# Performance work log

Hardware: AMD Instinct MI355X
Metric: run time of the kernel (lower is better)

Reference implementation:

```python
import jax, jax.numpy as jnp
import numpy as np

N = 100000
E = 3200000
D_IN = 256
D_OUT = 256
SMOOTH = 0.5


def setup_inputs() -> dict:
    key = jax.random.key(0)
    k1, k2, k3, k4, k5, k6 = jax.random.split(key, 6)
    x = jax.random.normal(k1, (N, D_IN), dtype=jnp.float32)
    W = jax.random.normal(k2, (D_IN, D_OUT), dtype=jnp.float32) * (1.0 / np.sqrt(D_IN))
    b = jax.random.normal(k3, (D_OUT,), dtype=jnp.float32) * 0.01
    edge_weight = jax.random.uniform(k4, (E,), dtype=jnp.float32)
    edge_row = jax.random.randint(k5, (E,), 0, N, dtype=jnp.int32)
    edge_col = jax.random.randint(k6, (E,), 0, N, dtype=jnp.int32)
    return {"x": x, "W": W, "b": b, "edge_weight": edge_weight,
            "edge_row": edge_row, "edge_col": edge_col}


def reference(x, W, b, edge_weight, edge_row, edge_col):
    # support = Linear(input)
    support = x @ W + b  # [N, D_OUT]
    # A_gcn = adj + I; degrees = column sums of A_gcn (identity contributes +1)
    deg = jax.ops.segment_sum(edge_weight, edge_col, num_segments=N) + 1.0  # [N]
    Dm12 = deg ** -0.5  # D^{-1/2}
    # pre-scale, spmm with A_gcn = adj + I, post-scale
    Y = support * Dm12[:, None]
    Z = jax.ops.segment_sum(edge_weight[:, None] * Y[edge_col], edge_row,
                            num_segments=N) + Y  # +Y is the identity part of A_gcn
    Z = Z * Dm12[:, None]
    # residual blend
    return (Z * SMOOTH + support) / (1.0 + SMOOTH)
```

## Files before the change

### kernel.cpp

```cpp
#include <hip/hip_runtime.h>

#define N_NODES 100000
#define N_EDGES 3200000
#define D 256
#define ELL_W 64
#define NPC_CNT 57344
#define NPART_CNT 2
#define NTOTC 114688
#define NPC_ELL 28672
#define NPART_ELL 4
#define NPC_DEG 57344
#define NPART_DEG 2
#define NSLICE2 128
#define SLICE2_E 25000
#define NSLICE_D 128
#define SLICE_D 25000
#define W_SCALE 32768.0f
#define SMOOTH_A (1.0f/3.0f)
#define SMOOTH_B (2.0f/3.0f)

#define AS1 __attribute__((address_space(1)))
#define AS3 __attribute__((address_space(3)))

typedef __attribute__((ext_vector_type(8))) __bf16 bf16x8;
typedef __attribute__((ext_vector_type(4))) float f32x4;
typedef __attribute__((ext_vector_type(2))) float f32x2;

__device__ __forceinline__ unsigned short f2bf(float f) {
    unsigned int u = __float_as_uint(f);
    u = (u + 0x7FFFu + ((u >> 16) & 1u)) >> 16;
    return (unsigned short)u;
}
__device__ __forceinline__ float bf_lo(unsigned int u) { return __uint_as_float(u << 16); }
__device__ __forceinline__ float bf_hi(unsigned int u) { return __uint_as_float(u & 0xFFFF0000u); }

__device__ __forceinline__ unsigned int cvtpk_bf16(float lo, float hi) {
    unsigned int r;
    asm("v_cvt_pk_bf16_f32 %0, %1, %2" : "=v"(r) : "v"(lo), "v"(hi));
    return r;
}

__device__ __forceinline__ void load_lds16(const void* g, void* l) {
    __builtin_amdgcn_global_load_lds((const AS1 unsigned int*)g, (AS3 unsigned int*)l, 16, 0, 0);
}

__global__ void prep_cw_kernel(const int* __restrict__ ecol, const float* __restrict__ ew,
                               unsigned int* __restrict__ cw) {
    int i = blockIdx.x * 256 + threadIdx.x;
    int e0 = i * 4;
    if (e0 >= N_EDGES) return;
    int4 c = *(const int4*)(ecol + e0);
    float4 w = *(const float4*)(ew + e0);
    uint4 o; unsigned q;
    q = __float2uint_rn(w.x * W_SCALE); if (q > 32767u) q = 32767u; o.x = (unsigned)c.x | (q << 17);
    q = __float2uint_rn(w.y * W_SCALE); if (q > 32767u) q = 32767u; o.y = (unsigned)c.y | (q << 17);
    q = __float2uint_rn(w.z * W_SCALE); if (q > 32767u) q = 32767u; o.z = (unsigned)c.z | (q << 17);
    q = __float2uint_rn(w.w * W_SCALE); if (q > 32767u) q = 32767u; o.w = (unsigned)c.w | (q << 17);
    *(uint4*)(cw + e0) = o;
}

__launch_bounds__(256, 2)
__global__ void cntpart_kernel(const int* __restrict__ erow, unsigned char* __restrict__ cnt_s) {
    __shared__ unsigned int h[NPC_CNT / 4];
    int p = blockIdx.x, s = blockIdx.y;
    int base = p * NPC_CNT;
    for (int i = threadIdx.x; i < NPC_CNT / 4; i += 256) h[i] = 0u;
    __syncthreads();
    int q0 = (s * SLICE2_E) >> 2, q1 = q0 + (SLICE2_E >> 2);
    const int4* r4p = (const int4*)erow;
    for (int q = q0 + threadIdx.x; q < q1; q += 256) {
        int4 r = r4p[q];
        int a;
        a = r.x - base; if ((unsigned)a < NPC_CNT) atomicAdd(&h[a >> 2], 1u << ((a & 3) * 8));
        a = r.y - base; if ((unsigned)a < NPC_CNT) atomicAdd(&h[a >> 2], 1u << ((a & 3) * 8));
        a = r.z - base; if ((unsigned)a < NPC_CNT) atomicAdd(&h[a >> 2], 1u << ((a & 3) * 8));
        a = r.w - base; if ((unsigned)a < NPC_CNT) atomicAdd(&h[a >> 2], 1u << ((a & 3) * 8));
    }
    __syncthreads();
    unsigned int* dst = (unsigned int*)(cnt_s + (size_t)s * NTOTC + base);
    for (int i = threadIdx.x; i < NPC_CNT / 4; i += 256) dst[i] = h[i];
}

__launch_bounds__(256, 2)
__global__ void degpart_kernel(const unsigned int* __restrict__ cw, unsigned char* __restrict__ degp) {
    __shared__ unsigned int h[NPC_DEG / 4];
    int p = blockIdx.x, s = blockIdx.y;
    int base = p * NPC_DEG;
    for (int i = threadIdx.x; i < NPC_DEG / 4; i += 256) h[i] = 0u;
    __syncthreads();
    int q0 = (s * SLICE_D) >> 2, q1 = q0 + (SLICE_D >> 2);
    const uint4* c4p = (const uint4*)cw;
    for (int q = q0 + threadIdx.x; q < q1; q += 256) {
        uint4 v = c4p[q];
        int a; unsigned qw;
        a = (int)(v.x & 0x1FFFFu) - base; qw = ((v.x >> 17) + 512u) >> 10;
        if ((unsigned)a < NPC_DEG) atomicAdd(&h[a >> 2], qw << ((a & 3) * 8));
        a = (int)(v.y & 0x1FFFFu) - base; qw = ((v.y >> 17) + 512u) >> 10;
        if ((unsigned)a < NPC_DEG) atomicAdd(&h[a >> 2], qw << ((a & 3) * 8));
        a = (int)(v.z & 0x1FFFFu) - base; qw = ((v.z >> 17) + 512u) >> 10;
        if ((unsigned)a < NPC_DEG) atomicAdd(&h[a >> 2], qw << ((a & 3) * 8));
        a = (int)(v.w & 0x1FFFFu) - base; qw = ((v.w >> 17) + 512u) >> 10;
        if ((unsigned)a < NPC_DEG) atomicAdd(&h[a >> 2], qw << ((a & 3) * 8));
    }
    __syncthreads();
    unsigned int* dst = (unsigned int*)(degp + (size_t)s * NTOTC + base);
    for (int i = threadIdx.x; i < NPC_DEG / 4; i += 256) dst[i] = h[i];
}

__global__ void scanboth_kernel(unsigned char* __restrict__ cnt_s, int* __restrict__ mcnt,
                                const unsigned char* __restrict__ degp, float* __restrict__ dm12) {
    int r = blockIdx.x * 256 + threadIdx.x;
    if (r >= NTOTC) return;
    unsigned int acc = 0;
#pragma unroll
    for (int s = 0; s < NSLICE2; s++) {
        unsigned int v = cnt_s[(size_t)s * NTOTC + r];
        cnt_s[(size_t)s * NTOTC + r] = (unsigned char)acc;
        acc += v;
    }
    mcnt[r] = (int)acc;
    unsigned int qsum = 0;
#pragma unroll
    for (int s = 0; s < NSLICE_D; s++)
        qsum += degp[(size_t)s * NTOTC + r];
    dm12[r] = rsqrtf(1.0f + (float)qsum * (1.0f / 32.0f));
}

__launch_bounds__(256, 4)
__global__ void ellwrite_kernel(const int* __restrict__ erow, const unsigned int* __restrict__ cw,
                                const unsigned char* __restrict__ off,
                                unsigned int* __restrict__ ell) {
    __shared__ unsigned int h[NPC_ELL / 4];
    int p = blockIdx.x, s = blockIdx.y;
    int base = p * NPC_ELL;
    for (int i = threadIdx.x; i < NPC_ELL / 4; i += 256) h[i] = 0u;
    __syncthreads();
    int q0 = (s * SLICE2_E) >> 2, q1 = q0 + (SLICE2_E >> 2);
    const int4* r4p = (const int4*)erow;
    const uint4* c4p = (const uint4*)cw;
    const unsigned char* offs = off + (size_t)s * NTOTC;
#define PUT(rr, vv) do { \
        int a_ = (rr) - base; \
        if ((unsigned)a_ < NPC_ELL) { \
            int sh_ = (a_ & 3) * 8; \
            unsigned int old_ = atomicAdd(&h[a_ >> 2], 1u << sh_); \
            unsigned int rank_ = (old_ >> sh_) & 0xFFu; \
            unsigned int pos_ = (unsigned int)offs[rr] + rank_; \
            if (pos_ < ELL_W) ell[(size_t)(rr) * ELL_W + pos_] = (vv); \
        } \
    } while (0)
    for (int q = q0 + threadIdx.x; q < q1; q += 256) {
        int4 r = r4p[q];
        uint4 v = c4p[q];
        PUT(r.x, v.x);
        PUT(r.y, v.y);
        PUT(r.z, v.z);
        PUT(r.w, v.w);
    }
#undef PUT
}

__global__ void cvt_wt_kernel(const float* __restrict__ W, unsigned short* __restrict__ wt) {
    int t = blockIdx.x * 256 + threadIdx.x;
    int c = t >> 8, k = t & 255;
    wt[t] = f2bf(W[k * D + c]);
}

__launch_bounds__(256, 4)
__global__ void gemm_kernel(const float* __restrict__ x,
                            const unsigned short* __restrict__ wt,
                            const float* __restrict__ bias, const float* __restrict__ dm12,
                            unsigned short* __restrict__ Yh, unsigned char* __restrict__ Yq,
                            int n) {
    __shared__ __align__(16) float As[128 * 32];
    __shared__ __align__(16) unsigned short Bs[128 * 32];
    int t = threadIdx.x;
    int lane = t & 63, wave = t >> 6;
    int wm = wave >> 1, wn = wave & 1;
    int r0 = blockIdx.x * 128;
    int c0 = blockIdx.y * 128;

    f32x4 zero4 = {0.f, 0.f, 0.f, 0.f};
    f32x4 acc[4][4];
#pragma unroll
    for (int m = 0; m < 4; m++)
#pragma unroll
        for (int nn = 0; nn < 4; nn++) acc[m][nn] = zero4;

    int srow = t >> 2;
    int bseg = (t & 3) ^ ((t >> 3) & 3);
    int skseg = bseg * 8;
    char* bbase = (char*)Bs + wave * 1024;
    int aseg = (lane & 7) ^ (lane >> 3);

    for (int kc = 0; kc < 256; kc += 32) {
#pragma unroll
        for (int i = 0; i < 4; i++) {
            int row_local = (i * 4 + wave) * 8 + (lane >> 3);
            int grow = r0 + row_local;
            if (grow >= n) grow = n - 1;
            load_lds16(x + (size_t)grow * 256 + kc + aseg * 4,
                       (char*)As + (i * 4 + wave) * 1024);
        }
        load_lds16(wt + (size_t)(c0 + srow) * 256 + kc + skseg,      bbase);
        load_lds16(wt + (size_t)(c0 + 64 + srow) * 256 + kc + skseg, bbase + 4096);
        __syncthreads();

        bf16x8 bfrag[4];
        bf16x8 afrag[4];
        int lr = lane & 15;
        int seg0 = (lane >> 4) * 2;
        int bsegr = lane >> 4;
#pragma unroll
        for (int m = 0; m < 4; m++) {
            int row = wm * 64 + m * 16 + lr;
            int rk = row & 7;
            const char* rbase = (const char*)As + row * 128;
            f32x4 a0 = *(const f32x4*)(rbase + ((seg0 ^ rk) << 4));
            f32x4 a1 = *(const f32x4*)(rbase + (((seg0 + 1) ^ rk) << 4));
            union { bf16x8 v; unsigned int u[4]; } af;
            af.u[0] = cvtpk_bf16(a0.x, a0.y);
            af.u[1] = cvtpk_bf16(a0.z, a0.w);
            af.u[2] = cvtpk_bf16(a1.x, a1.y);
            af.u[3] = cvtpk_bf16(a1.z, a1.w);
            afrag[m] = af.v;
        }
#pragma unroll
        for (int nn = 0; nn < 4; nn++) {
            int row = wn * 64 + nn * 16 + lr;
            int rk = (row >> 1) & 3;
            bfrag[nn] = *(const bf16x8*)((const char*)Bs + row * 64 + ((bsegr ^ rk) << 4));
        }
#pragma unroll
        for (int m = 0; m < 4; m++)
#pragma unroll
            for (int nn = 0; nn < 4; nn++)
                acc[m][nn] = __builtin_amdgcn_mfma_f32_16x16x32_bf16(bfrag[nn], afrag[m], acc[m][nn], 0, 0, 0);
        __syncthreads();
    }

#pragma unroll
    for (int m = 0; m < 4; m++) {
        int r = r0 + wm * 64 + m * 16 + (lane & 15);
        if (r < n) {
            float dm = dm12[r];
#pragma unroll
            for (int nn = 0; nn < 4; nn++) {
                int colbase = c0 + wn * 64 + nn * 16 + (lane >> 4) * 4;
                float4 b4 = *(const float4*)(bias + colbase);
                f32x4 v = acc[m][nn];
                float v0 = (v[0] + b4.x) * dm;
                float v1 = (v[1] + b4.y) * dm;
                float v2 = (v[2] + b4.z) * dm;
                float v3 = (v[3] + b4.w) * dm;
                uint2 hv;
                hv.x = cvtpk_bf16(v0, v1);
                hv.y = cvtpk_bf16(v2, v3);
                *(uint2*)(Yh + (size_t)r * 256 + colbase) = hv;
                int q = 0;
                q = __builtin_amdgcn_cvt_pk_fp8_f32(v0, v1, q, false);
                q = __builtin_amdgcn_cvt_pk_fp8_f32(v2, v3, q, true);
                *(unsigned int*)(Yq + (size_t)r * 256 + colbase) = (unsigned int)q;
            }
        }
    }
}

__launch_bounds__(256)
__global__ void gather_kernel(const unsigned short* __restrict__ Yh,
                              const unsigned int* __restrict__ Yq,
                              const int* __restrict__ cnt, const unsigned int* __restrict__ ell,
                              const float* __restrict__ dm12, float* __restrict__ out, int n) {
    int wid = threadIdx.x >> 6, lane = threadIdx.x & 63;
    int r = __builtin_amdgcn_readfirstlane(blockIdx.x * 4 + wid);
    if (r >= n) return;
    const uint2* Y2 = (const uint2*)Yh;
    uint2 ow = Y2[(size_t)r * 64 + lane];
    float o0 = bf_lo(ow.x), o1 = bf_hi(ow.x), o2 = bf_lo(ow.y), o3 = bf_hi(ow.y);
    float a0 = o0, a1 = o1, a2 = o2, a3 = o3;
    int m = cnt[r]; if (m > ELL_W) m = ELL_W;
    const uint4* ep4 = (const uint4*)(ell + (size_t)r * ELL_W);
    int j = 0;
#define WDEC(v) ((float)((v) >> 17) * (1.0f / W_SCALE))
#define CDEC(v) ((v) & 0x1FFFFu)
#define EDGE(qreg, wreg) do { \
        f32x2 lo_ = __builtin_amdgcn_cvt_pk_f32_fp8((int)(qreg), false); \
        f32x2 hi_ = __builtin_amdgcn_cvt_pk_f32_fp8((int)(qreg), true);  \
        a0 = fmaf((wreg), lo_.x, a0); a1 = fmaf((wreg), lo_.y, a1);      \
        a2 = fmaf((wreg), hi_.x, a2); a3 = fmaf((wreg), hi_.y, a3);      \
    } while (0)
    for (; j + 15 < m; j += 16) {
        uint4 eA = ep4[(j >> 2) + 0];
        uint4 eB = ep4[(j >> 2) + 1];
        uint4 eC = ep4[(j >> 2) + 2];
        uint4 eD = ep4[(j >> 2) + 3];
        unsigned int q0  = Yq[(size_t)CDEC(eA.x) * 64 + lane];
        unsigned int q1  = Yq[(size_t)CDEC(eA.y) * 64 + lane];
        unsigned int q2  = Yq[(size_t)CDEC(eA.z) * 64 + lane];
        unsigned int q3  = Yq[(size_t)CDEC(eA.w) * 64 + lane];
        unsigned int q4  = Yq[(size_t)CDEC(eB.x) * 64 + lane];
        unsigned int q5  = Yq[(size_t)CDEC(eB.y) * 64 + lane];
        unsigned int q6  = Yq[(size_t)CDEC(eB.z) * 64 + lane];
        unsigned int q7  = Yq[(size_t)CDEC(eB.w) * 64 + lane];
        unsigned int q8  = Yq[(size_t)CDEC(eC.x) * 64 + lane];
        unsigned int q9  = Yq[(size_t)CDEC(eC.y) * 64 + lane];
        unsigned int q10 = Yq[(size_t)CDEC(eC.z) * 64 + lane];
        unsigned int q11 = Yq[(size_t)CDEC(eC.w) * 64 + lane];
        unsigned int q12 = Yq[(size_t)CDEC(eD.x) * 64 + lane];
        unsigned int q13 = Yq[(size_t)CDEC(eD.y) * 64 + lane];
        unsigned int q14 = Yq[(size_t)CDEC(eD.z) * 64 + lane];
        unsigned int q15 = Yq[(size_t)CDEC(eD.w) * 64 + lane];
        EDGE(q0,  WDEC(eA.x)); EDGE(q1,  WDEC(eA.y));
        EDGE(q2,  WDEC(eA.z)); EDGE(q3,  WDEC(eA.w));
        EDGE(q4,  WDEC(eB.x)); EDGE(q5,  WDEC(eB.y));
        EDGE(q6,  WDEC(eB.z)); EDGE(q7,  WDEC(eB.w));
        EDGE(q8,  WDEC(eC.x)); EDGE(q9,  WDEC(eC.y));
        EDGE(q10, WDEC(eC.z)); EDGE(q11, WDEC(eC.w));
        EDGE(q12, WDEC(eD.x)); EDGE(q13, WDEC(eD.y));
        EDGE(q14, WDEC(eD.z)); EDGE(q15, WDEC(eD.w));
    }
    for (; j + 7 < m; j += 8) {
        uint4 eA = ep4[(j >> 2) + 0];
        uint4 eB = ep4[(j >> 2) + 1];
        unsigned int q0 = Yq[(size_t)CDEC(eA.x) * 64 + lane];
        unsigned int q1 = Yq[(size_t)CDEC(eA.y) * 64 + lane];
        unsigned int q2 = Yq[(size_t)CDEC(eA.z) * 64 + lane];
        unsigned int q3 = Yq[(size_t)CDEC(eA.w) * 64 + lane];
        unsigned int q4 = Yq[(size_t)CDEC(eB.x) * 64 + lane];
        unsigned int q5 = Yq[(size_t)CDEC(eB.y) * 64 + lane];
        unsigned int q6 = Yq[(size_t)CDEC(eB.z) * 64 + lane];
        unsigned int q7 = Yq[(size_t)CDEC(eB.w) * 64 + lane];
        EDGE(q0, WDEC(eA.x)); EDGE(q1, WDEC(eA.y));
        EDGE(q2, WDEC(eA.z)); EDGE(q3, WDEC(eA.w));
        EDGE(q4, WDEC(eB.x)); EDGE(q5, WDEC(eB.y));
        EDGE(q6, WDEC(eB.z)); EDGE(q7, WDEC(eB.w));
    }
    for (; j + 3 < m; j += 4) {
        uint4 eA = ep4[j >> 2];
        unsigned int q0 = Yq[(size_t)CDEC(eA.x) * 64 + lane];
        unsigned int q1 = Yq[(size_t)CDEC(eA.y) * 64 + lane];
        unsigned int q2 = Yq[(size_t)CDEC(eA.z) * 64 + lane];
        unsigned int q3 = Yq[(size_t)CDEC(eA.w) * 64 + lane];
        EDGE(q0, WDEC(eA.x)); EDGE(q1, WDEC(eA.y));
        EDGE(q2, WDEC(eA.z)); EDGE(q3, WDEC(eA.w));
    }
    for (; j < m; j++) {
        unsigned int ev = ell[(size_t)r * ELL_W + j];
        unsigned int qa = Yq[(size_t)CDEC(ev) * 64 + lane];
        EDGE(qa, WDEC(ev));
    }
#undef EDGE
#undef WDEC
#undef CDEC
    float dm = dm12[r];
    float inv = 1.0f / dm;
    float4 o;
    o.x = (a0 * dm) * SMOOTH_A + (o0 * inv) * SMOOTH_B;
    o.y = (a1 * dm) * SMOOTH_A + (o1 * inv) * SMOOTH_B;
    o.z = (a2 * dm) * SMOOTH_A + (o2 * inv) * SMOOTH_B;
    o.w = (a3 * dm) * SMOOTH_A + (o3 * inv) * SMOOTH_B;
    ((float4*)out)[(size_t)r * 64 + lane] = o;
}

extern "C" void kernel_launch(void* const* d_in, const int* in_sizes, int n_in,
                              void* d_out, int out_size, void* d_ws, size_t ws_size,
                              hipStream_t stream) {
    const float* x    = (const float*)d_in[0];
    const float* W    = (const float*)d_in[1];
    const float* b    = (const float*)d_in[2];
    const float* ew   = (const float*)d_in[3];
    const int*   erow = (const int*)d_in[4];
    const int*   ecol = (const int*)d_in[5];
    float* out = (float*)d_out;
    const int n = N_NODES;

    char* wp = (char*)d_ws;
    int*   mcnt = (int*)wp;   wp += 458752;
    float* dm12 = (float*)wp; wp += 458752;
    unsigned short* wt = (unsigned short*)wp; wp += 131072;
    unsigned int* cw = (unsigned int*)wp; wp += (size_t)N_EDGES * 4;
    unsigned int* ell = (unsigned int*)wp; wp += (size_t)N_NODES * ELL_W * 4;
    char*  rgA  = wp;         wp += (size_t)n * D * 2;
    unsigned short* Yh    = (unsigned short*)rgA;
    unsigned char*  cnt_s = (unsigned char*)rgA;
    char*  rgB  = wp;
    unsigned char* degp = (unsigned char*)rgB;
    unsigned char* Yq   = (unsigned char*)rgB;

    prep_cw_kernel<<<(N_EDGES / 4 + 255) / 256, 256, 0, stream>>>(ecol, ew, cw);
    cntpart_kernel<<<dim3(NPART_CNT, NSLICE2), 256, 0, stream>>>(erow, cnt_s);
    degpart_kernel<<<dim3(NPART_DEG, NSLICE_D), 256, 0, stream>>>(cw, degp);
    scanboth_kernel<<<(NTOTC + 255) / 256, 256, 0, stream>>>(cnt_s, mcnt, degp, dm12);
    ellwrite_kernel<<<dim3(NPART_ELL, NSLICE2), 256, 0, stream>>>(erow, cw, cnt_s, ell);
    cvt_wt_kernel<<<(D * D) / 256, 256, 0, stream>>>(W, wt);
    gemm_kernel<<<dim3(782, 2), 256, 0, stream>>>(x, wt, b, dm12, Yh, Yq, n);
    gather_kernel<<<(n + 3) / 4, 256, 0, stream>>>(Yh, (const unsigned int*)Yq, mcnt, ell, dm12, out, n);
}
```

Measured before the change: 316.2 us.

## Sort ELL rows by column and gather in column phases across multiple rows

Adds a per-row bitonic sort of ELL entries by column plus a phase table of column-range boundaries. The gather kernel now has each wave process 13 rows, sweeping 16 column phases so concurrent gathers touch a narrower region of the fp8 feature table for better cache reuse. This costs an extra sort pass over the ELL array, less memory-level parallelism per row, and higher register pressure from 13 accumulator sets.

After: 857.4 us. 171% more time.

```diff
diff --git a/kernel.cpp b/kernel.cpp
--- a/kernel.cpp
+++ b/kernel.cpp
@@ -16,6 +16,10 @@
 #define NSLICE_D 128
 #define SLICE_D 25000
 #define W_SCALE 32768.0f
+#define NPHASE 16
+#define PHASE_W 6250
+#define ROWS_PW 13
+#define PG_BLOCKS 1924
 #define SMOOTH_A (1.0f/3.0f)
 #define SMOOTH_B (2.0f/3.0f)
 
@@ -160,6 +164,36 @@
 #undef PUT
 }
 
+__launch_bounds__(256)
+__global__ void ellsort_kernel(unsigned int* __restrict__ ell, const int* __restrict__ mcnt,
+                               unsigned char* __restrict__ ptab, int n) {
+    int wid = threadIdx.x >> 6, lane = threadIdx.x & 63;
+    int r = blockIdx.x * 4 + wid;
+    if (r >= n) return;
+    int m = mcnt[r]; if (m > ELL_W) m = ELL_W;
+    unsigned int v = (lane < m) ? ell[(size_t)r * ELL_W + lane] : 0u;
+    unsigned int key = (lane < m) ? ((v << 15) | (v >> 17)) : 0xFFFFFFFFu;
+#pragma unroll
+    for (int k = 2; k <= 64; k <<= 1) {
+#pragma unroll
+        for (int j = k >> 1; j > 0; j >>= 1) {
+            unsigned int other = (unsigned int)__shfl_xor((int)key, j, 64);
+            bool dirUp = ((lane & k) == 0);
+            bool iAmLow = ((lane & j) == 0);
+            unsigned int mn = key < other ? key : other;
+            unsigned int mx = key < other ? other : key;
+            key = (dirUp == iAmLow) ? mn : mx;
+        }
+    }
+    unsigned int col = key >> 15;
+    for (int p = 0; p < NPHASE; p++) {
+        unsigned long long bal = __ballot(col < (unsigned)((p + 1) * PHASE_W));
+        int c = __popcll(bal);
+        if (lane == p) ptab[(size_t)r * NPHASE + p] = (unsigned char)c;
+    }
+    if (lane < m) ell[(size_t)r * ELL_W + lane] = (key >> 15) | (key << 17);
+}
+
 __global__ void cvt_wt_kernel(const float* __restrict__ W, unsigned short* __restrict__ wt) {
     int t = blockIdx.x * 256 + threadIdx.x;
     int c = t >> 8, k = t & 255;
@@ -267,99 +301,75 @@
 }
 
 __launch_bounds__(256)
-__global__ void gather_kernel(const unsigned short* __restrict__ Yh,
-                              const unsigned int* __restrict__ Yq,
-                              const int* __restrict__ cnt, const unsigned int* __restrict__ ell,
-                              const float* __restrict__ dm12, float* __restrict__ out, int n) {
+__global__ void pgather_kernel(const unsigned short* __restrict__ Yh,
+                               const unsigned int* __restrict__ Yq,
+                               const unsigned int* __restrict__ ell,
+                               const unsigned char* __restrict__ ptab,
+                               const float* __restrict__ dm12, float* __restrict__ out, int n) {
     int wid = threadIdx.x >> 6, lane = threadIdx.x & 63;
-    int r = __builtin_amdgcn_readfirstlane(blockIdx.x * 4 + wid);
-    if (r >= n) return;
-    const uint2* Y2 = (const uint2*)Yh;
-    uint2 ow = Y2[(size_t)r * 64 + lane];
-    float o0 = bf_lo(ow.x), o1 = bf_hi(ow.x), o2 = bf_lo(ow.y), o3 = bf_hi(ow.y);
-    float a0 = o0, a1 = o1, a2 = o2, a3 = o3;
-    int m = cnt[r]; if (m > ELL_W) m = ELL_W;
-    const uint4* ep4 = (const uint4*)(ell + (size_t)r * ELL_W);
-    int j = 0;
+    int rbase = (blockIdx.x * 4 + wid) * ROWS_PW;
+    if (rbase >= n) return;
+
+    f32x4 acc[ROWS_PW];
+#pragma unroll
+    for (int i = 0; i < ROWS_PW; i++) acc[i] = (f32x4){0.f, 0.f, 0.f, 0.f};
+
 #define WDEC(v) ((float)((v) >> 17) * (1.0f / W_SCALE))
 #define CDEC(v) ((v) & 0x1FFFFu)
-#define EDGE(qreg, wreg) do { \
-        f32x2 lo_ = __builtin_amdgcn_cvt_pk_f32_fp8((int)(qreg), false); \
-        f32x2 hi_ = __builtin_amdgcn_cvt_pk_f32_fp8((int)(qreg), true);  \
-        a0 = fmaf((wreg), lo_.x, a0); a1 = fmaf((wreg), lo_.y, a1);      \
-        a2 = fmaf((wreg), hi_.x, a2); a3 = fmaf((wreg), hi_.y, a3);      \
-    } while (0)
-    for (; j + 15 < m; j += 16) {
-        uint4 eA = ep4[(j >> 2) + 0];
-        uint4 eB = ep4[(j >> 2) + 1];
-        uint4 eC = ep4[(j >> 2) + 2];
-        uint4 eD = ep4[(j >> 2) + 3];
-        unsigned int q0  = Yq[(size_t)CDEC(eA.x) * 64 + lane];
-        unsigned int q1  = Yq[(size_t)CDEC(eA.y) * 64 + lane];
-        unsigned int q2  = Yq[(size_t)CDEC(eA.z) * 64 + lane];
-        unsigned int q3  = Yq[(size_t)CDEC(eA.w) * 64 + lane];
-        unsigned int q4  = Yq[(size_t)CDEC(eB.x) * 64 + lane];
-        unsigned int q5  = Yq[(size_t)CDEC(eB.y) * 64 + lane];
-        unsigned int q6  = Yq[(size_t)CDEC(eB.z) * 64 + lane];
-        unsigned int q7  = Yq[(size_t)CDEC(eB.w) * 64 + lane];
-        unsigned int q8  = Yq[(size_t)CDEC(eC.x) * 64 + lane];
-        unsigned int q9  = Yq[(size_t)CDEC(eC.y) * 64 + lane];
-        unsigned int q10 = Yq[(size_t)CDEC(eC.z) * 64 + lane];
-        unsigned int q11 = Yq[(size_t)CDEC(eC.w) * 64 + lane];
-        unsigned int q12 = Yq[(size_t)CDEC(eD.x) * 64 + lane];
-        unsigned int q13 = Yq[(size_t)CDEC(eD.y) * 64 + lane];
-        unsigned int q14 = Yq[(size_t)CDEC(eD.z) * 64 + lane];
-        unsigned int q15 = Yq[(size_t)CDEC(eD.w) * 64 + lane];
-        EDGE(q0,  WDEC(eA.x)); EDGE(q1,  WDEC(eA.y));
-        EDGE(q2,  WDEC(eA.z)); EDGE(q3,  WDEC(eA.w));
-        EDGE(q4,  WDEC(eB.x)); EDGE(q5,  WDEC(eB.y));
-        EDGE(q6,  WDEC(eB.z)); EDGE(q7,  WDEC(eB.w));
-        EDGE(q8,  WDEC(eC.x)); EDGE(q9,  WDEC(eC.y));
-        EDGE(q10, WDEC(eC.z)); EDGE(q11, WDEC(eC.w));
-        EDGE(q12, WDEC(eD.x)); EDGE(q13, WDEC(eD.y));
-        EDGE(q14, WDEC(eD.z)); EDGE(q15, WDEC(eD.w));
-    }
-    for (; j + 7 < m; j += 8) {
-        uint4 eA = ep4[(j >> 2) + 0];
-        uint4 eB = ep4[(j >> 2) + 1];
-        unsigned int q0 = Yq[(size_t)CDEC(eA.x) * 64 + lane];
-        unsigned int q1 = Yq[(size_t)CDEC(eA.y) * 64 + lane];
-        unsigned int q2 = Yq[(size_t)CDEC(eA.z) * 64 + lane];
-        unsigned int q3 = Yq[(size_t)CDEC(eA.w) * 64 + lane];
-        unsigned int q4 = Yq[(size_t)CDEC(eB.x) * 64 + lane];
-        unsigned int q5 = Yq[(size_t)CDEC(eB.y) * 64 + lane];
-        unsigned int q6 = Yq[(size_t)CDEC(eB.z) * 64 + lane];
-        unsigned int q7 = Yq[(size_t)CDEC(eB.w) * 64 + lane];
-        EDGE(q0, WDEC(eA.x)); EDGE(q1, WDEC(eA.y));
-        EDGE(q2, WDEC(eA.z)); EDGE(q3, WDEC(eA.w));
-        EDGE(q4, WDEC(eB.x)); EDGE(q5, WDEC(eB.y));
-        EDGE(q6, WDEC(eB.z)); EDGE(q7, WDEC(eB.w));
-    }
-    for (; j + 3 < m; j += 4) {
-        uint4 eA = ep4[j >> 2];
-        unsigned int q0 = Yq[(size_t)CDEC(eA.x) * 64 + lane];
-        unsigned int q1 = Yq[(size_t)CDEC(eA.y) * 64 + lane];
-        unsigned int q2 = Yq[(size_t)CDEC(eA.z) * 64 + lane];
-        unsigned int q3 = Yq[(size_t)CDEC(eA.w) * 64 + lane];
-        EDGE(q0, WDEC(eA.x)); EDGE(q1, WDEC(eA.y));
-        EDGE(q2, WDEC(eA.z)); EDGE(q3, WDEC(eA.w));
-    }
-    for (; j < m; j++) {
-        unsigned int ev = ell[(size_t)r * ELL_W + j];
-        unsigned int qa = Yq[(size_t)CDEC(ev) * 64 + lane];
-        EDGE(qa, WDEC(ev));
-    }
-#undef EDGE
+    for (int cp = 0; cp < NPHASE; cp++) {
+#pragma unroll
+        for (int i = 0; i < ROWS_PW; i++) {
+            int r = rbase + i;
+            if (r >= n) continue;
+            const unsigned char* tb = ptab + (size_t)r * NPHASE;
+            int s_ = (cp == 0) ? 0 : (int)tb[cp - 1];
+            int e_ = (int)tb[cp];
+            const unsigned int* er = ell + (size_t)r * ELL_W;
+            int e = s_;
+            for (; e + 1 < e_; e += 2) {
+                unsigned int v0 = er[e], v1 = er[e + 1];
+                unsigned int q0 = Yq[(size_t)CDEC(v0) * 64 + lane];
+                unsigned int q1 = Yq[(size_t)CDEC(v1) * 64 + lane];
+                float w0 = WDEC(v0), w1 = WDEC(v1);
+                f32x2 l0 = __builtin_amdgcn_cvt_pk_f32_fp8((int)q0, false);
+                f32x2 h0 = __builtin_amdgcn_cvt_pk_f32_fp8((int)q0, true);
+                f32x2 l1 = __builtin_amdgcn_cvt_pk_f32_fp8((int)q1, false);
+                f32x2 h1 = __builtin_amdgcn_cvt_pk_f32_fp8((int)q1, true);
+                acc[i][0] = fmaf(w0, l0.x, acc[i][0]); acc[i][1] = fmaf(w0, l0.y, acc[i][1]);
+                acc[i][2] = fmaf(w0, h0.x, acc[i][2]); acc[i][3] = fmaf(w0, h0.y, acc[i][3]);
+                acc[i][0] = fmaf(w1, l1.x, acc[i][0]); acc[i][1] = fmaf(w1, l1.y, acc[i][1]);
+                acc[i][2] = fmaf(w1, h1.x, acc[i][2]); acc[i][3] = fmaf(w1, h1.y, acc[i][3]);
+            }
+            if (e < e_) {
+                unsigned int v0 = er[e];
+                unsigned int q0 = Yq[(size_t)CDEC(v0) * 64 + lane];
+                float w0 = WDEC(v0);
+                f32x2 l0 = __builtin_amdgcn_cvt_pk_f32_fp8((int)q0, false);
+                f32x2 h0 = __builtin_amdgcn_cvt_pk_f32_fp8((int)q0, true);
+                acc[i][0] = fmaf(w0, l0.x, acc[i][0]); acc[i][1] = fmaf(w0, l0.y, acc[i][1]);
+                acc[i][2] = fmaf(w0, h0.x, acc[i][2]); acc[i][3] = fmaf(w0, h0.y, acc[i][3]);
+            }
+        }
+    }
 #undef WDEC
 #undef CDEC
-    float dm = dm12[r];
-    float inv = 1.0f / dm;
-    float4 o;
-    o.x = (a0 * dm) * SMOOTH_A + (o0 * inv) * SMOOTH_B;
-    o.y = (a1 * dm) * SMOOTH_A + (o1 * inv) * SMOOTH_B;
-    o.z = (a2 * dm) * SMOOTH_A + (o2 * inv) * SMOOTH_B;
-    o.w = (a3 * dm) * SMOOTH_A + (o3 * inv) * SMOOTH_B;
-    ((float4*)out)[(size_t)r * 64 + lane] = o;
+
+    const uint2* Y2 = (const uint2*)Yh;
+#pragma unroll
+    for (int i = 0; i < ROWS_PW; i++) {
+        int r = rbase + i;
+        if (r >= n) continue;
+        uint2 ow = Y2[(size_t)r * 64 + lane];
+        float o0 = bf_lo(ow.x), o1 = bf_hi(ow.x), o2 = bf_lo(ow.y), o3 = bf_hi(ow.y);
+        float dm = dm12[r];
+        float inv = 1.0f / dm;
+        float4 o;
+        o.x = ((acc[i][0] + o0) * dm) * SMOOTH_A + (o0 * inv) * SMOOTH_B;
+        o.y = ((acc[i][1] + o1) * dm) * SMOOTH_A + (o1 * inv) * SMOOTH_B;
+        o.z = ((acc[i][2] + o2) * dm) * SMOOTH_A + (o2 * inv) * SMOOTH_B;
+        o.w = ((acc[i][3] + o3) * dm) * SMOOTH_A + (o3 * inv) * SMOOTH_B;
+        ((float4*)out)[(size_t)r * 64 + lane] = o;
+    }
 }
 
 extern "C" void kernel_launch(void* const* d_in, const int* in_sizes, int n_in,
@@ -380,6 +390,7 @@
     unsigned short* wt = (unsigned short*)wp; wp += 131072;
     unsigned int* cw = (unsigned int*)wp; wp += (size_t)N_EDGES * 4;
     unsigned int* ell = (unsigned int*)wp; wp += (size_t)N_NODES * ELL_W * 4;
+    unsigned char* ptab = (unsigned char*)wp; wp += (size_t)N_NODES * NPHASE;
     char*  rgA  = wp;         wp += (size_t)n * D * 2;
     unsigned short* Yh    = (unsigned short*)rgA;
     unsigned char*  cnt_s = (unsigned char*)rgA;
@@ -392,7 +403,8 @@
     degpart_kernel<<<dim3(NPART_DEG, NSLICE_D), 256, 0, stream>>>(cw, degp);
     scanboth_kernel<<<(NTOTC + 255) / 256, 256, 0, stream>>>(cnt_s, mcnt, degp, dm12);
     ellwrite_kernel<<<dim3(NPART_ELL, NSLICE2), 256, 0, stream>>>(erow, cw, cnt_s, ell);
+    ellsort_kernel<<<(n + 3) / 4, 256, 0, stream>>>(ell, mcnt, ptab, n);
     cvt_wt_kernel<<<(D * D) / 256, 256, 0, stream>>>(W, wt);
     gemm_kernel<<<dim3(782, 2), 256, 0, stream>>>(x, wt, b, dm12, Yh, Yq, n);
-    gather_kernel<<<(n + 3) / 4, 256, 0, stream>>>(Yh, (const unsigned int*)Yq, mcnt, ell, dm12, out, n);
-}
+    pgather_kernel<<<PG_BLOCKS, 256, 0, stream>>>(Yh, (const unsigned int*)Yq, ell, ptab, dm12, out, n);
+}
```
